# Kernel tuning notes

Hardware: AMD Instinct MI355X
Metric: run time of the kernel (lower is better)

## Reference

```python
import jax, jax.numpy as jnp
import numpy as np

N = 50000        # nodes
E = 1600000      # edges
G = 512          # graphs in batch
IN = 128         # in_dim
HID = 32         # hidden_dim
H = 4            # heads in conv1
NEG_SLOPE = 0.2  # PyG GATConv default


def setup_inputs() -> dict:
    key = jax.random.key(0)
    ks = jax.random.split(key, 20)
    s = 0.05
    return {
        "x": jax.random.normal(ks[0], (N, IN), jnp.float32),
        "edge_index": jax.random.randint(ks[1], (2, E), 0, N, dtype=jnp.int64),
        "edge_attr": jax.random.normal(ks[2], (E, 8), jnp.float32),
        "batch": jnp.sort(jax.random.randint(ks[3], (N,), 0, G, dtype=jnp.int64)),
        # conv1: in=IN, out=HID, heads=H, concat=True
        "W1": jax.random.normal(ks[4], (IN, H * HID), jnp.float32) * s,
        "a_src1": jax.random.normal(ks[5], (H, HID), jnp.float32) * s,
        "a_dst1": jax.random.normal(ks[6], (H, HID), jnp.float32) * s,
        "b1": jnp.zeros((H * HID,), jnp.float32),
        # conv2: in=H*HID, out=HID, heads=1, concat=False
        "W2": jax.random.normal(ks[7], (H * HID, HID), jnp.float32) * s,
        "a_src2": jax.random.normal(ks[8], (1, HID), jnp.float32) * s,
        "a_dst2": jax.random.normal(ks[9], (1, HID), jnp.float32) * s,
        "b2": jnp.zeros((HID,), jnp.float32),
        # classifier: HID -> HID//2 -> 1
        "Wc1": jax.random.normal(ks[10], (HID, HID // 2), jnp.float32) * s,
        "bc1": jnp.zeros((HID // 2,), jnp.float32),
        "Wc2": jax.random.normal(ks[11], (HID // 2, 1), jnp.float32) * s,
        "bc2": jnp.zeros((1,), jnp.float32),
    }


def gat_layer(x, src, dst, W, a_src, a_dst, b, heads, ch, concat, n):
    """PyG GATConv (eval mode): linear, edge-gathered additive attention,
    per-destination segment softmax, scatter-add aggregation."""
    h = (x @ W).reshape(n, heads, ch)                       # [N,H,C]
    alpha_s = jnp.sum(h * a_src, axis=-1)                   # [N,H]
    alpha_d = jnp.sum(h * a_dst, axis=-1)                   # [N,H]
    e = jax.nn.leaky_relu(alpha_s[src] + alpha_d[dst], NEG_SLOPE)  # [Etot,H]
    m = jax.lax.stop_gradient(jax.ops.segment_max(e, dst, num_segments=n))
    ex = jnp.exp(e - m[dst])
    den = jax.ops.segment_sum(ex, dst, num_segments=n)      # [N,H]
    alpha = ex / den[dst]                                   # [Etot,H]
    out = jax.ops.segment_sum(alpha[:, :, None] * h[src], dst, num_segments=n)
    out = out.reshape(n, heads * ch) if concat else out.mean(axis=1)
    return out + b


def reference(x, edge_index, edge_attr, batch,
              W1, a_src1, a_dst1, b1,
              W2, a_src2, a_dst2, b2,
              Wc1, bc1, Wc2, bc2):
    # add self-loops (PyG GATConv default)
    loop = jnp.arange(N, dtype=edge_index.dtype)
    src = jnp.concatenate([edge_index[0], loop])
    dst = jnp.concatenate([edge_index[1], loop])

    h = jax.nn.elu(gat_layer(x, src, dst, W1, a_src1, a_dst1, b1, H, HID, True, N))
    h = jax.nn.elu(gat_layer(h, src, dst, W2, a_src2, a_dst2, b2, 1, HID, False, N))

    # global mean pool over graphs
    cnt = jax.ops.segment_sum(jnp.ones((N,), h.dtype), batch, num_segments=G)
    pooled = jax.ops.segment_sum(h, batch, num_segments=G) / cnt[:, None]

    z = jax.nn.relu(pooled @ Wc1 + bc1)
    return (z @ Wc2 + bc2).squeeze(-1)   # [G]
```

## Files before the change

kernel.cpp:

```cpp
#include <hip/hip_runtime.h>
#include <math.h>

#define BUCKET_SHIFT 7
#define BUCKET_NODES (1 << BUCKET_SHIFT)
#define MAX_BUCK 512
#define PART_CHUNK 8192
#define PART_EPT 32

typedef _Float16 half4v __attribute__((ext_vector_type(4)));
typedef _Float16 half8v __attribute__((ext_vector_type(8)));

__device__ __forceinline__ float leaky02(float x){ return x > 0.f ? x : 0.2f * x; }
__device__ __forceinline__ float eluf(float x){ return x > 0.f ? x : expm1f(x); }

__global__ __launch_bounds__(256) void gemm1_hist_kernel(
    const float* __restrict__ x, const float* __restrict__ W,
    const float* __restrict__ a_src, const float* __restrict__ a_dst,
    _Float16* __restrict__ h, float* __restrict__ as_, float* __restrict__ ad_, int n,
    const int* __restrict__ dstv, int* __restrict__ bucketPartial, int pbPad,
    int E, int K, int histBlocks,
    int* __restrict__ zbase, int zwords)
{
  const int t = threadIdx.x;
  if (blockIdx.x < histBlocks) {
    __shared__ int hist[MAX_BUCK];
    for (int b = t; b < K; b += 256) hist[b] = 0;
    __syncthreads();
    const int j = blockIdx.x;
    int cbase = j * PART_CHUNK;
    for (int q = 0; q < PART_EPT; ++q) {
      int e = cbase + q * 256 + t;
      if (e < E) atomicAdd(&hist[dstv[e] >> BUCKET_SHIFT], 1);
    }
    __syncthreads();
    for (int b = t; b < K; b += 256)
      bucketPartial[(size_t)b * pbPad + j] = hist[b];
    if (j == 0) {
      for (int i = t; i < zwords; i += 256) zbase[i] = 0;
    }
    return;
  }
  const int g = blockIdx.x - histBlocks;
  const int row0 = g * 16;
  __shared__ float xs[16][128];
  __shared__ float sS[16][128];
  __shared__ float sD[16][128];
  for (int idx = t; idx < 16 * 32; idx += 256) {
    int r = idx >> 5, k4 = idx & 31;
    float4 v = (row0 + r < n) ? ((const float4*)x)[(size_t)(row0 + r) * 32 + k4]
                              : make_float4(0.f, 0.f, 0.f, 0.f);
    *(float4*)&xs[r][k4 * 4] = v;
  }
  __syncthreads();
  const int col = t & 127, hf = t >> 7;
  float acc[8] = {0,0,0,0,0,0,0,0};
  for (int k = 0; k < 128; k += 4) {
    float w0 = W[(k + 0) * 128 + col];
    float w1 = W[(k + 1) * 128 + col];
    float w2 = W[(k + 2) * 128 + col];
    float w3 = W[(k + 3) * 128 + col];
    #pragma unroll
    for (int r = 0; r < 8; ++r) {
      const float4 xv = *(const float4*)&xs[hf * 8 + r][k];
      acc[r] += xv.x * w0 + xv.y * w1 + xv.z * w2 + xv.w * w3;
    }
  }
  float asv = a_src[col], adv = a_dst[col];
  #pragma unroll
  for (int r = 0; r < 8; ++r) {
    int row = hf * 8 + r;
    float hv = acc[r];
    if (row0 + row < n) h[(size_t)(row0 + row) * 128 + col] = (_Float16)hv;
    sS[row][col] = hv * asv;
    sD[row][col] = hv * adv;
  }
  __syncthreads();
  if (t < 128) {
    int r = t >> 3, head = (t >> 1) & 3, which = t & 1;
    if (row0 + r < n) {
      const float (*buf)[128] = which ? sD : sS;
      double s2 = 0;
      for (int cc = 0; cc < 32; ++cc) s2 += (double)buf[r][head * 32 + cc];
      (which ? ad_ : as_)[(row0 + r) * 4 + head] = (float)s2;
    }
  }
}

__global__ __launch_bounds__(256) void scan_rows_kernel(
    int* __restrict__ partial, int pbPad, int* __restrict__ bucketStart, int pb)
{
  const int b = blockIdx.x;
  const int t = threadIdx.x;
  int* row = partial + (size_t)b * pbPad;
  __shared__ int s[256];
  __shared__ int carry_s;
  if (t == 0) carry_s = 0;
  __syncthreads();
  for (int base = 0; base < pb; base += 256) {
    int v = (base + t < pb) ? row[base + t] : 0;
    s[t] = v;
    __syncthreads();
    for (int off = 1; off < 256; off <<= 1) {
      int xv = (t >= off) ? s[t - off] : 0;
      __syncthreads();
      s[t] += xv;
      __syncthreads();
    }
    int incl = s[t];
    int carry = carry_s;
    if (base + t < pb) row[base + t] = carry + incl - v;
    __syncthreads();
    if (t == 255) carry_s = carry + incl;
    __syncthreads();
  }
  if (t == 0) bucketStart[b] = carry_s;
}

__global__ __launch_bounds__(256) void scan_buckets_kernel(int* __restrict__ arr, int nb) {
  __shared__ int s[256];
  __shared__ int carry_s;
  int t = threadIdx.x;
  if (t == 0) carry_s = 0;
  __syncthreads();
  for (int b = 0; b < nb; b += 256) {
    int v = (b + t < nb) ? arr[b + t] : 0;
    s[t] = v;
    __syncthreads();
    for (int off = 1; off < 256; off <<= 1) {
      int x = (t >= off) ? s[t - off] : 0;
      __syncthreads();
      s[t] += x;
      __syncthreads();
    }
    int incl = s[t];
    int carry = carry_s;
    if (b + t < nb) arr[b + t] = carry + incl - v;
    __syncthreads();
    if (t == 255) carry_s = carry + incl;
    __syncthreads();
  }
}

__global__ __launch_bounds__(256) void partition_kernel(
    const int* __restrict__ src, const int* __restrict__ dst,
    const int* __restrict__ bucketStart, const int* __restrict__ pre, int pbPad,
    unsigned int* __restrict__ bucketed, int E, int K)
{
  __shared__ int base_s[MAX_BUCK];
  __shared__ int cur[MAX_BUCK];
  const int j = blockIdx.x;
  for (int b = threadIdx.x; b < K; b += 256) {
    base_s[b] = bucketStart[b] + pre[(size_t)b * pbPad + j];
    cur[b] = 0;
  }
  __syncthreads();
  int cbase = j * PART_CHUNK;
  for (int q = 0; q < PART_EPT; ++q) {
    int e = cbase + q * 256 + threadIdx.x;
    if (e < E) {
      int d = dst[e];
      int b = d >> BUCKET_SHIFT;
      int r = atomicAdd(&cur[b], 1);
      bucketed[base_s[b] + r] =
          ((unsigned int)src[e] << BUCKET_SHIFT) | (unsigned int)(d & (BUCKET_NODES - 1));
    }
  }
}

__global__ __launch_bounds__(256) void fill_csr_kernel(
    const unsigned int* __restrict__ bucketed, const int* __restrict__ bucketStart,
    int* __restrict__ rowStart, int* __restrict__ col, int n, int E, int K)
{
  int b = blockIdx.x;
  int nodeBase = b << BUCKET_SHIFT;
  int t = threadIdx.x;
  __shared__ int hist[BUCKET_NODES];
  __shared__ int rs[BUCKET_NODES];
  __shared__ int cur[BUCKET_NODES];
  if (t < BUCKET_NODES) hist[t] = 0;
  __syncthreads();
  int bs = bucketStart[b];
  int be = (b + 1 < K) ? bucketStart[b + 1] : E;
  for (int i = bs + t; i < be; i += 256)
    atomicAdd(&hist[bucketed[i] & (BUCKET_NODES - 1)], 1);
  __syncthreads();
  if (t < BUCKET_NODES) rs[t] = hist[t];
  __syncthreads();
  for (int off = 1; off < BUCKET_NODES; off <<= 1) {
    int v = (t < BUCKET_NODES && t >= off) ? rs[t - off] : 0;
    __syncthreads();
    if (t < BUCKET_NODES) rs[t] += v;
    __syncthreads();
  }
  if (t < BUCKET_NODES) {
    int node = nodeBase + t;
    int excl = bs + rs[t] - hist[t];
    if (node < n) rowStart[node] = excl;
    rs[t] = excl;
    cur[t] = 0;
  }
  if (b == K - 1 && t == 0) rowStart[n] = E;
  __syncthreads();
  for (int i = bs + t; i < be; i += 256) {
    unsigned int rec = bucketed[i];
    int local = rec & (BUCKET_NODES - 1);
    int pos = rs[local] + atomicAdd(&cur[local], 1);
    col[pos] = (int)(rec >> BUCKET_SHIFT);
  }
}

__global__ __launch_bounds__(256) void gat_aggr1_kernel(
    const _Float16* __restrict__ feat,
    const float* __restrict__ as_,
    const float* __restrict__ ad_,
    const int* __restrict__ rowStart,
    const int* __restrict__ col,
    const float* __restrict__ bias,
    _Float16* __restrict__ out, int n)
{
  constexpr int CHUNK = 16;
  const int t    = threadIdx.x;
  const int wave = t >> 6;
  const int lane = t & 63;
  const int grp  = lane >> 4;
  const int li   = lane & 15;
  const int slot = wave * 4 + grp;
  const int node = blockIdx.x * 16 + slot;
  const int hc   = li >> 2;

  __shared__ int   s_off[16][CHUNK];
  __shared__ float s_p[16][CHUNK * 4];

  if (node >= n) return;

  const int beg = rowStart[node];
  const int deg = rowStart[node + 1] - beg;

  const float4 advv = ((const float4*)ad_)[node];
  const float4 asvv = ((const float4*)as_)[node];
  const float adv[4] = {advv.x, advv.y, advv.z, advv.w};
  float es;
  {
    float e0 = leaky02(asvv.x + adv[0]);
    float e1 = leaky02(asvv.y + adv[1]);
    float e2 = leaky02(asvv.z + adv[2]);
    float e3 = leaky02(asvv.w + adv[3]);
    es = (hc == 0) ? e0 : (hc == 1) ? e1 : (hc == 2) ? e2 : e3;
  }
  const float ps = expf(es);

  const char* featc = (const char*)feat + (li << 4);
  const half8v fself = *(const half8v*)(featc + ((size_t)node << 8));
  float accf[8];
  #pragma unroll
  for (int q = 0; q < 8; ++q) accf[q] = ps * (float)fself[q];
  float den = ps;

  int    st_s = 0;
  float4 st_q = make_float4(0.f, 0.f, 0.f, 0.f);
  if (deg > 0 && li < min(CHUNK, deg)) {
    st_s = col[beg + li];
    st_q = ((const float4*)as_)[st_s];
  }

  const int nch = (deg + CHUNK - 1) / CHUNK;
  for (int c = 0; c < nch; ++c) {
    const int base = c * CHUNK;
    const int cnt  = min(CHUNK, deg - base);
    if (li < cnt) {
      s_off[slot][li] = st_s << 8;
      float4 pp;
      pp.x = expf(leaky02(st_q.x + adv[0]));
      pp.y = expf(leaky02(st_q.y + adv[1]));
      pp.z = expf(leaky02(st_q.z + adv[2]));
      pp.w = expf(leaky02(st_q.w + adv[3]));
      *(float4*)&s_p[slot][li * 4] = pp;
    }
    __builtin_amdgcn_wave_barrier();
    const int nbase = base + CHUNK;
    if (nbase + li < deg) {
      st_s = col[beg + nbase + li];
      st_q = ((const float4*)as_)[st_s];
    }
    float a[8] = {0,0,0,0,0,0,0,0};
    float df = 0.f;
    if (cnt == CHUNK) {
      int off[16];
      #pragma unroll
      for (int j = 0; j < 16; ++j) off[j] = s_off[slot][j];
      half8v r[16];
      #pragma unroll
      for (int j = 0; j < 16; ++j) r[j] = *(const half8v*)(featc + off[j]);
      #pragma unroll
      for (int j = 0; j < 16; ++j) {
        float p = s_p[slot][j * 4 + hc];
        #pragma unroll
        for (int q = 0; q < 8; ++q) a[q] += p * (float)r[j][q];
        df += p;
      }
    } else {
      for (int j = 0; j < cnt; ++j) {
        int off = s_off[slot][j];
        float p = s_p[slot][j * 4 + hc];
        const half8v f = *(const half8v*)(featc + off);
        #pragma unroll
        for (int q = 0; q < 8; ++q) a[q] += p * (float)f[q];
        df += p;
      }
    }
    __builtin_amdgcn_wave_barrier();
    #pragma unroll
    for (int q = 0; q < 8; ++q) accf[q] += a[q];
    den += df;
  }

  const float4 bv0 = ((const float4*)bias)[2 * li];
  const float4 bv1 = ((const float4*)bias)[2 * li + 1];
  const float bb[8] = {bv0.x, bv0.y, bv0.z, bv0.w, bv1.x, bv1.y, bv1.z, bv1.w};
  const float inv = 1.0f / den;
  half8v ov;
  #pragma unroll
  for (int q = 0; q < 8; ++q)
    ov[q] = (_Float16)eluf(accf[q] * inv + bb[q]);
  *(half8v*)((char*)out + ((size_t)node << 8) + (li << 4)) = ov;
}

__global__ __launch_bounds__(128) void gemm2_kernel(
    const _Float16* __restrict__ x, const float* __restrict__ W,
    const float* __restrict__ a_src, const float* __restrict__ a_dst,
    _Float16* __restrict__ h, float* __restrict__ as_, float* __restrict__ ad_, int n)
{
  const int t = threadIdx.x;
  const int row0 = blockIdx.x * 8;
  __shared__ float xs[8][128];
  __shared__ float sH[8][32];
  for (int idx = t; idx < 8 * 16; idx += 128) {
    int r = idx >> 4, k8 = idx & 15;
    half8v v;
    #pragma unroll
    for (int q = 0; q < 8; ++q) v[q] = (_Float16)0.f;
    if (row0 + r < n) v = ((const half8v*)x)[(size_t)(row0 + r) * 16 + k8];
    #pragma unroll
    for (int q = 0; q < 8; ++q) xs[r][k8 * 8 + q] = (float)v[q];
  }
  __syncthreads();
  int col = t & 31, rp = t >> 5;
  int r0 = rp * 2, r1 = r0 + 1;
  float a0 = 0, a1 = 0;
  for (int k = 0; k < 128; k += 4) {
    float w0 = W[(k + 0) * 32 + col];
    float w1 = W[(k + 1) * 32 + col];
    float w2 = W[(k + 2) * 32 + col];
    float w3 = W[(k + 3) * 32 + col];
    float4 x0 = *(const float4*)&xs[r0][k];
    float4 x1 = *(const float4*)&xs[r1][k];
    a0 += x0.x * w0 + x0.y * w1 + x0.z * w2 + x0.w * w3;
    a1 += x1.x * w0 + x1.y * w1 + x1.z * w2 + x1.w * w3;
  }
  if (row0 + r0 < n) h[(size_t)(row0 + r0) * 32 + col] = (_Float16)a0;
  if (row0 + r1 < n) h[(size_t)(row0 + r1) * 32 + col] = (_Float16)a1;
  sH[r0][col] = a0; sH[r1][col] = a1;
  __syncthreads();
  if (t < 16) {
    int r = t >> 1, which = t & 1;
    if (row0 + r < n) {
      const float* a = which ? a_dst : a_src;
      double s = 0;
      for (int cc = 0; cc < 32; ++cc) s += (double)sH[r][cc] * (double)a[cc];
      (which ? ad_ : as_)[row0 + r] = (float)s;
    }
  }
}

__global__ __launch_bounds__(256) void gat_aggr2_kernel(
    const _Float16* __restrict__ feat,
    const float* __restrict__ as_,
    const float* __restrict__ ad_,
    const int* __restrict__ rowStart,
    const int* __restrict__ col,
    const float* __restrict__ bias,
    float* __restrict__ out, int n)
{
  constexpr int CHUNK = 16;
  const int t    = threadIdx.x;
  const int wave = t >> 6;
  const int lane = t & 63;
  const int grp  = lane >> 3;
  const int li   = lane & 7;
  const int slot = wave * 8 + grp;
  const int node = blockIdx.x * 32 + slot;

  __shared__ int   s_off[32][CHUNK];
  __shared__ float s_p[32][CHUNK];

  if (node >= n) return;

  const int beg = rowStart[node];
  const int deg = rowStart[node + 1] - beg;

  const float adv = ad_[node];
  const float ps  = expf(leaky02(as_[node] + adv));

  const char* featc = (const char*)feat + (li << 3);
  const half4v fself = *(const half4v*)(featc + ((size_t)node << 6));
  float a0s = ps * (float)fself.x;
  float a1s = ps * (float)fself.y;
  float a2s = ps * (float)fself.z;
  float a3s = ps * (float)fself.w;
  float den = ps;

  int   st_s0 = 0, st_s1 = 0;
  float st_q0 = 0.f, st_q1 = 0.f;
  if (deg > 0) {
    int c0 = min(CHUNK, deg);
    if (li < c0)     { st_s0 = col[beg + li];     st_q0 = as_[st_s0]; }
    if (li + 8 < c0) { st_s1 = col[beg + li + 8]; st_q1 = as_[st_s1]; }
  }

  const int nch = (deg + CHUNK - 1) / CHUNK;
  for (int c = 0; c < nch; ++c) {
    const int base = c * CHUNK;
    const int cnt  = min(CHUNK, deg - base);
    if (li < cnt)     { s_off[slot][li]     = st_s0 << 6; s_p[slot][li]     = expf(leaky02(st_q0 + adv)); }
    if (li + 8 < cnt) { s_off[slot][li + 8] = st_s1 << 6; s_p[slot][li + 8] = expf(leaky02(st_q1 + adv)); }
    __builtin_amdgcn_wave_barrier();
    const int nbase = base + CHUNK;
    if (nbase < deg) {
      if (nbase + li < deg)     { st_s0 = col[beg + nbase + li];     st_q0 = as_[st_s0]; }
      if (nbase + li + 8 < deg) { st_s1 = col[beg + nbase + li + 8]; st_q1 = as_[st_s1]; }
    }
    float a0 = 0.f, a1 = 0.f, a2 = 0.f, a3 = 0.f, df = 0.f;
    if (cnt == CHUNK) {
      int off[16];
      #pragma unroll
      for (int j = 0; j < 16; ++j) off[j] = s_off[slot][j];
      half4v r[16];
      #pragma unroll
      for (int j = 0; j < 16; ++j) r[j] = *(const half4v*)(featc + off[j]);
      #pragma unroll
      for (int j = 0; j < 16; ++j) {
        float p = s_p[slot][j];
        a0 += p * (float)r[j].x; a1 += p * (float)r[j].y;
        a2 += p * (float)r[j].z; a3 += p * (float)r[j].w;
        df += p;
      }
    } else {
      for (int j = 0; j < cnt; ++j) {
        int off = s_off[slot][j];
        float p = s_p[slot][j];
        const half4v f = *(const half4v*)(featc + off);
        a0 += p * (float)f.x; a1 += p * (float)f.y;
        a2 += p * (float)f.z; a3 += p * (float)f.w;
        df += p;
      }
    }
    __builtin_amdgcn_wave_barrier();
    a0s += a0; a1s += a1; a2s += a2; a3s += a3;
    den += df;
  }

  const float inv = 1.0f / den;
  const float4 bv = *(const float4*)(bias + 4 * li);
  float4 o;
  o.x = eluf(a0s * inv + bv.x);
  o.y = eluf(a1s * inv + bv.y);
  o.z = eluf(a2s * inv + bv.z);
  o.w = eluf(a3s * inv + bv.w);
  *(float4*)(out + (size_t)node * 32 + 4 * li) = o;
}

__global__ __launch_bounds__(256) void pool_kernel(const float* __restrict__ act2,
    const int* __restrict__ batch, float* __restrict__ pooled,
    float* __restrict__ cnt, int n)
{
  int t = threadIdx.x;
  int c = t & 31, r = t >> 5;
  int n0 = blockIdx.x * 64 + r * 8;
  float run = 0.f; int gcur = -1; int len = 0;
  for (int i = 0; i < 8; ++i) {
    int nd = n0 + i;
    if (nd >= n) break;
    int gb = batch[nd];
    if (gb != gcur) {
      if (gcur >= 0) {
        atomicAdd(&pooled[gcur * 32 + c], run);
        if (c == 0) atomicAdd(&cnt[gcur], (float)len);
      }
      gcur = gb; run = 0.f; len = 0;
    }
    run += act2[(size_t)nd * 32 + c];
    len++;
  }
  if (gcur >= 0) {
    atomicAdd(&pooled[gcur * 32 + c], run);
    if (c == 0) atomicAdd(&cnt[gcur], (float)len);
  }
}

__global__ void classifier_kernel(const float* __restrict__ pooled, const float* __restrict__ cnt,
    const float* __restrict__ Wc1, const float* __restrict__ bc1,
    const float* __restrict__ Wc2, const float* __restrict__ bc2,
    float* __restrict__ outp, int g_total)
{
  int g = blockIdx.x * blockDim.x + threadIdx.x;
  if (g < g_total) {
    float inv = 1.0f / cnt[g];
    float pm[32];
    for (int c = 0; c < 32; ++c) pm[c] = pooled[g * 32 + c] * inv;
    double o = (double)bc2[0];
    for (int j = 0; j < 16; ++j) {
      double z = (double)bc1[j];
      for (int c = 0; c < 32; ++c) z += (double)pm[c] * (double)Wc1[c * 16 + j];
      float zr = (float)z;
      zr = zr > 0.f ? zr : 0.f;
      o += (double)zr * (double)Wc2[j];
    }
    outp[g] = (float)o;
  }
}

extern "C" void kernel_launch(void* const* d_in, const int* in_sizes, int n_in,
                              void* d_out, int out_size, void* d_ws, size_t ws_size,
                              hipStream_t stream)
{
  const float* x      = (const float*)d_in[0];
  const int*   ei     = (const int*)d_in[1];
  const int*   batch  = (const int*)d_in[3];
  const float* W1     = (const float*)d_in[4];
  const float* a_src1 = (const float*)d_in[5];
  const float* a_dst1 = (const float*)d_in[6];
  const float* b1     = (const float*)d_in[7];
  const float* W2     = (const float*)d_in[8];
  const float* a_src2 = (const float*)d_in[9];
  const float* a_dst2 = (const float*)d_in[10];
  const float* b2     = (const float*)d_in[11];
  const float* Wc1    = (const float*)d_in[12];
  const float* bc1    = (const float*)d_in[13];
  const float* Wc2    = (const float*)d_in[14];
  const float* bc2    = (const float*)d_in[15];

  const int N = in_sizes[0] / 128;
  const int E = in_sizes[1] / 2;
  const int G = out_size;

  const int* srcv = ei;
  const int* dstv = ei + E;

  char* ws = (char*)d_ws;
  size_t off = 0;
  auto alloc = [&](size_t bytes) -> void* {
    void* p = ws + off;
    off += (bytes + 255) & ~(size_t)255;
    return p;
  };
  const int K  = (N + BUCKET_NODES - 1) >> BUCKET_SHIFT;
  const int pb = (E + PART_CHUNK - 1) / PART_CHUNK;
  const int pbPad = (pb + 63) & ~63;

  _Float16* h1   = (_Float16*)alloc((size_t)N * 128 * 2);
  _Float16* act1 = (_Float16*)alloc((size_t)N * 128 * 2);
  _Float16* h2   = (_Float16*)alloc((size_t)N * 32 * 2);
  float* act2  = (float*)alloc((size_t)N * 32 * 4);
  float* as1   = (float*)alloc((size_t)N * 4 * 4);
  float* ad1   = (float*)alloc((size_t)N * 4 * 4);
  float* as2   = (float*)alloc((size_t)N * 4);
  float* ad2   = (float*)alloc((size_t)N * 4);
  int*   rowStart = (int*)alloc((size_t)(N + 1) * 4);
  int*   colv     = (int*)alloc((size_t)E * 4);
  unsigned int* bucketed = (unsigned int*)alloc((size_t)E * 4);
  int*   bucketPartial = (int*)alloc((size_t)MAX_BUCK * pbPad * 4);
  int*   bucketStart   = (int*)alloc((size_t)MAX_BUCK * 4);
  size_t zoff0 = off;
  float* pooled = (float*)alloc((size_t)G * 32 * 4);
  float* cntG   = (float*)alloc((size_t)G * 4);
  size_t zoff1 = off;
  const int zwords = (int)((zoff1 - zoff0) / 4);
  int* zbase = (int*)pooled;

  const int gemmBlocks = (N + 15) / 16;
  gemm1_hist_kernel<<<pb + gemmBlocks, 256, 0, stream>>>(
      x, W1, a_src1, a_dst1, h1, as1, ad1, N,
      dstv, bucketPartial, pbPad, E, K, pb, zbase, zwords);
  scan_rows_kernel<<<K, 256, 0, stream>>>(bucketPartial, pbPad, bucketStart, pb);
  scan_buckets_kernel<<<1, 256, 0, stream>>>(bucketStart, K);
  partition_kernel<<<pb, 256, 0, stream>>>(srcv, dstv, bucketStart, bucketPartial, pbPad,
                                           bucketed, E, K);
  fill_csr_kernel<<<K, 256, 0, stream>>>(bucketed, bucketStart, rowStart, colv, N, E, K);
  gat_aggr1_kernel<<<(N + 15) / 16, 256, 0, stream>>>(h1, as1, ad1, rowStart, colv, b1, act1, N);
  gemm2_kernel<<<(N + 7) / 8, 128, 0, stream>>>(act1, W2, a_src2, a_dst2, h2, as2, ad2, N);
  gat_aggr2_kernel<<<(N + 31) / 32, 256, 0, stream>>>(h2, as2, ad2, rowStart, colv, b2, act2, N);
  pool_kernel<<<(N + 63) / 64, 256, 0, stream>>>(act2, batch, pooled, cntG, N);
  classifier_kernel<<<(G + 255) / 256, 256, 0, stream>>>(pooled, cntG, Wc1, bc1, Wc2, bc2,
                                                         (float*)d_out, G);
}
```

Baseline: 364.1 us.

## Fuse bucket scan into partition/fill kernels and double aggregation chunk size

Removes the single-block scan_buckets_kernel launch; each partition and fill_csr block now recomputes the exclusive scan of bucket totals in LDS. Both GAT aggregation kernels double their edge chunk from 16 to 32 and prefetch twice as many neighbor indices and attention scores per iteration. The scan change trades one serial launch for redundant per-block scan work. The larger chunk puts more gather loads in flight per step, at the cost of register and LDS pressure and more partial chunks for low-degree nodes.

```diff
diff --git a/kernel.cpp b/kernel.cpp
--- a/kernel.cpp
+++ b/kernel.cpp
@@ -12,6 +12,29 @@
 
 __device__ __forceinline__ float leaky02(float x){ return x > 0.f ? x : 0.2f * x; }
 __device__ __forceinline__ float eluf(float x){ return x > 0.f ? x : expm1f(x); }
+
+__device__ __forceinline__ void lds_exclusive_scan(int* sc, int K, int* s, int* carry_s) {
+  const int t = threadIdx.x;
+  if (t == 0) *carry_s = 0;
+  __syncthreads();
+  for (int base = 0; base < K; base += 256) {
+    int v = (base + t < K) ? sc[base + t] : 0;
+    s[t] = v;
+    __syncthreads();
+    for (int off = 1; off < 256; off <<= 1) {
+      int xv = (t >= off) ? s[t - off] : 0;
+      __syncthreads();
+      s[t] += xv;
+      __syncthreads();
+    }
+    int incl = s[t];
+    int carry = *carry_s;
+    if (base + t < K) sc[base + t] = carry + incl - v;
+    __syncthreads();
+    if (t == 255) *carry_s = carry + incl;
+    __syncthreads();
+  }
+}
 
 __global__ __launch_bounds__(256) void gemm1_hist_kernel(
     const float* __restrict__ x, const float* __restrict__ W,
@@ -87,7 +110,7 @@
 }
 
 __global__ __launch_bounds__(256) void scan_rows_kernel(
-    int* __restrict__ partial, int pbPad, int* __restrict__ bucketStart, int pb)
+    int* __restrict__ partial, int pbPad, int* __restrict__ bucketTotal, int pb)
 {
   const int b = blockIdx.x;
   const int t = threadIdx.x;
@@ -113,50 +136,32 @@
     if (t == 255) carry_s = carry + incl;
     __syncthreads();
   }
-  if (t == 0) bucketStart[b] = carry_s;
-}
-
-__global__ __launch_bounds__(256) void scan_buckets_kernel(int* __restrict__ arr, int nb) {
+  if (t == 0) bucketTotal[b] = carry_s;
+}
+
+__global__ __launch_bounds__(256) void partition_kernel(
+    const int* __restrict__ src, const int* __restrict__ dst,
+    const int* __restrict__ bucketTotal, const int* __restrict__ pre, int pbPad,
+    unsigned int* __restrict__ bucketed, int E, int K)
+{
+  __shared__ int sc[MAX_BUCK];
   __shared__ int s[256];
   __shared__ int carry_s;
-  int t = threadIdx.x;
-  if (t == 0) carry_s = 0;
-  __syncthreads();
-  for (int b = 0; b < nb; b += 256) {
-    int v = (b + t < nb) ? arr[b + t] : 0;
-    s[t] = v;
-    __syncthreads();
-    for (int off = 1; off < 256; off <<= 1) {
-      int x = (t >= off) ? s[t - off] : 0;
-      __syncthreads();
-      s[t] += x;
-      __syncthreads();
-    }
-    int incl = s[t];
-    int carry = carry_s;
-    if (b + t < nb) arr[b + t] = carry + incl - v;
-    __syncthreads();
-    if (t == 255) carry_s = carry + incl;
-    __syncthreads();
-  }
-}
-
-__global__ __launch_bounds__(256) void partition_kernel(
-    const int* __restrict__ src, const int* __restrict__ dst,
-    const int* __restrict__ bucketStart, const int* __restrict__ pre, int pbPad,
-    unsigned int* __restrict__ bucketed, int E, int K)
-{
   __shared__ int base_s[MAX_BUCK];
   __shared__ int cur[MAX_BUCK];
+  const int t = threadIdx.x;
   const int j = blockIdx.x;
-  for (int b = threadIdx.x; b < K; b += 256) {
-    base_s[b] = bucketStart[b] + pre[(size_t)b * pbPad + j];
+  for (int b = t; b < K; b += 256) sc[b] = bucketTotal[b];
+  __syncthreads();
+  lds_exclusive_scan(sc, K, s, &carry_s);
+  for (int b = t; b < K; b += 256) {
+    base_s[b] = sc[b] + pre[(size_t)b * pbPad + j];
     cur[b] = 0;
   }
   __syncthreads();
   int cbase = j * PART_CHUNK;
   for (int q = 0; q < PART_EPT; ++q) {
-    int e = cbase + q * 256 + threadIdx.x;
+    int e = cbase + q * 256 + t;
     if (e < E) {
       int d = dst[e];
       int b = d >> BUCKET_SHIFT;
@@ -168,19 +173,24 @@
 }
 
 __global__ __launch_bounds__(256) void fill_csr_kernel(
-    const unsigned int* __restrict__ bucketed, const int* __restrict__ bucketStart,
+    const unsigned int* __restrict__ bucketed, const int* __restrict__ bucketTotal,
     int* __restrict__ rowStart, int* __restrict__ col, int n, int E, int K)
 {
   int b = blockIdx.x;
   int nodeBase = b << BUCKET_SHIFT;
   int t = threadIdx.x;
+  __shared__ int sc[MAX_BUCK];
+  __shared__ int s[256];
+  __shared__ int carry_s;
   __shared__ int hist[BUCKET_NODES];
   __shared__ int rs[BUCKET_NODES];
   __shared__ int cur[BUCKET_NODES];
+  for (int bb = t; bb < K; bb += 256) sc[bb] = bucketTotal[bb];
   if (t < BUCKET_NODES) hist[t] = 0;
   __syncthreads();
-  int bs = bucketStart[b];
-  int be = (b + 1 < K) ? bucketStart[b + 1] : E;
+  lds_exclusive_scan(sc, K, s, &carry_s);
+  int bs = sc[b];
+  int be = (b + 1 < K) ? sc[b + 1] : E;
   for (int i = bs + t; i < be; i += 256)
     atomicAdd(&hist[bucketed[i] & (BUCKET_NODES - 1)], 1);
   __syncthreads();
@@ -218,7 +228,7 @@
     const float* __restrict__ bias,
     _Float16* __restrict__ out, int n)
 {
-  constexpr int CHUNK = 16;
+  constexpr int CHUNK = 32;
   const int t    = threadIdx.x;
   const int wave = t >> 6;
   const int lane = t & 63;
@@ -256,11 +266,13 @@
   for (int q = 0; q < 8; ++q) accf[q] = ps * (float)fself[q];
   float den = ps;
 
-  int    st_s = 0;
-  float4 st_q = make_float4(0.f, 0.f, 0.f, 0.f);
-  if (deg > 0 && li < min(CHUNK, deg)) {
-    st_s = col[beg + li];
-    st_q = ((const float4*)as_)[st_s];
+  int    st_s0 = 0, st_s1 = 0;
+  float4 st_q0 = make_float4(0.f, 0.f, 0.f, 0.f);
+  float4 st_q1 = make_float4(0.f, 0.f, 0.f, 0.f);
+  if (deg > 0) {
+    int c0 = min(CHUNK, deg);
+    if (li < c0)      { st_s0 = col[beg + li];      st_q0 = ((const float4*)as_)[st_s0]; }
+    if (li + 16 < c0) { st_s1 = col[beg + li + 16]; st_q1 = ((const float4*)as_)[st_s1]; }
   }
 
   const int nch = (deg + CHUNK - 1) / CHUNK;
@@ -268,35 +280,51 @@
     const int base = c * CHUNK;
     const int cnt  = min(CHUNK, deg - base);
     if (li < cnt) {
-      s_off[slot][li] = st_s << 8;
+      s_off[slot][li] = st_s0 << 8;
       float4 pp;
-      pp.x = expf(leaky02(st_q.x + adv[0]));
-      pp.y = expf(leaky02(st_q.y + adv[1]));
-      pp.z = expf(leaky02(st_q.z + adv[2]));
-      pp.w = expf(leaky02(st_q.w + adv[3]));
+      pp.x = expf(leaky02(st_q0.x + adv[0]));
+      pp.y = expf(leaky02(st_q0.y + adv[1]));
+      pp.z = expf(leaky02(st_q0.z + adv[2]));
+      pp.w = expf(leaky02(st_q0.w + adv[3]));
       *(float4*)&s_p[slot][li * 4] = pp;
+    }
+    if (li + 16 < cnt) {
+      s_off[slot][li + 16] = st_s1 << 8;
+      float4 pp;
+      pp.x = expf(leaky02(st_q1.x + adv[0]));
+      pp.y = expf(leaky02(st_q1.y + adv[1]));
+      pp.z = expf(leaky02(st_q1.z + adv[2]));
+      pp.w = expf(leaky02(st_q1.w + adv[3]));
+      *(float4*)&s_p[slot][(li + 16) * 4] = pp;
     }
     __builtin_amdgcn_wave_barrier();
     const int nbase = base + CHUNK;
     if (nbase + li < deg) {
-      st_s = col[beg + nbase + li];
-      st_q = ((const float4*)as_)[st_s];
+      st_s0 = col[beg + nbase + li];
+      st_q0 = ((const float4*)as_)[st_s0];
+    }
+    if (nbase + li + 16 < deg) {
+      st_s1 = col[beg + nbase + li + 16];
+      st_q1 = ((const float4*)as_)[st_s1];
     }
     float a[8] = {0,0,0,0,0,0,0,0};
     float df = 0.f;
     if (cnt == CHUNK) {
-      int off[16];
       #pragma unroll
-      for (int j = 0; j < 16; ++j) off[j] = s_off[slot][j];
-      half8v r[16];
-      #pragma unroll
-      for (int j = 0; j < 16; ++j) r[j] = *(const half8v*)(featc + off[j]);
-      #pragma unroll
-      for (int j = 0; j < 16; ++j) {
-        float p = s_p[slot][j * 4 + hc];
+      for (int half = 0; half < 2; ++half) {
+        int off[16];
         #pragma unroll
-        for (int q = 0; q < 8; ++q) a[q] += p * (float)r[j][q];
-        df += p;
+        for (int j = 0; j < 16; ++j) off[j] = s_off[slot][half * 16 + j];
+        half8v r[16];
+        #pragma unroll
+        for (int j = 0; j < 16; ++j) r[j] = *(const half8v*)(featc + off[j]);
+        #pragma unroll
+        for (int j = 0; j < 16; ++j) {
+          float p = s_p[slot][(half * 16 + j) * 4 + hc];
+          #pragma unroll
+          for (int q = 0; q < 8; ++q) a[q] += p * (float)r[j][q];
+          df += p;
+        }
       }
     } else {
       for (int j = 0; j < cnt; ++j) {
@@ -381,7 +409,7 @@
     const float* __restrict__ bias,
     float* __restrict__ out, int n)
 {
-  constexpr int CHUNK = 16;
+  constexpr int CHUNK = 32;
   const int t    = threadIdx.x;
   const int wave = t >> 6;
   const int lane = t & 63;
@@ -409,40 +437,49 @@
   float a3s = ps * (float)fself.w;
   float den = ps;
 
-  int   st_s0 = 0, st_s1 = 0;
-  float st_q0 = 0.f, st_q1 = 0.f;
+  int   st_s0 = 0, st_s1 = 0, st_s2 = 0, st_s3 = 0;
+  float st_q0 = 0.f, st_q1 = 0.f, st_q2 = 0.f, st_q3 = 0.f;
   if (deg > 0) {
     int c0 = min(CHUNK, deg);
-    if (li < c0)     { st_s0 = col[beg + li];     st_q0 = as_[st_s0]; }
-    if (li + 8 < c0) { st_s1 = col[beg + li + 8]; st_q1 = as_[st_s1]; }
+    if (li < c0)      { st_s0 = col[beg + li];      st_q0 = as_[st_s0]; }
+    if (li + 8 < c0)  { st_s1 = col[beg + li + 8];  st_q1 = as_[st_s1]; }
+    if (li + 16 < c0) { st_s2 = col[beg + li + 16]; st_q2 = as_[st_s2]; }
+    if (li + 24 < c0) { st_s3 = col[beg + li + 24]; st_q3 = as_[st_s3]; }
   }
 
   const int nch = (deg + CHUNK - 1) / CHUNK;
   for (int c = 0; c < nch; ++c) {
     const int base = c * CHUNK;
     const int cnt  = min(CHUNK, deg - base);
-    if (li < cnt)     { s_off[slot][li]     = st_s0 << 6; s_p[slot][li]     = expf(leaky02(st_q0 + adv)); }
-    if (li + 8 < cnt) { s_off[slot][li + 8] = st_s1 << 6; s_p[slot][li + 8] = expf(leaky02(st_q1 + adv)); }
+    if (li < cnt)      { s_off[slot][li]      = st_s0 << 6; s_p[slot][li]      = expf(leaky02(st_q0 + adv)); }
+    if (li + 8 < cnt)  { s_off[slot][li + 8]  = st_s1 << 6; s_p[slot][li + 8]  = expf(leaky02(st_q1 + adv)); }
+    if (li + 16 < cnt) { s_off[slot][li + 16] = st_s2 << 6; s_p[slot][li + 16] = expf(leaky02(st_q2 + adv)); }
+    if (li + 24 < cnt) { s_off[slot][li + 24] = st_s3 << 6; s_p[slot][li + 24] = expf(leaky02(st_q3 + adv)); }
     __builtin_amdgcn_wave_barrier();
     const int nbase = base + CHUNK;
     if (nbase < deg) {
-      if (nbase + li < deg)     { st_s0 = col[beg + nbase + li];     st_q0 = as_[st_s0]; }
-      if (nbase + li + 8 < deg) { st_s1 = col[beg + nbase + li + 8]; st_q1 = as_[st_s1]; }
+      if (nbase + li < deg)      { st_s0 = col[beg + nbase + li];      st_q0 = as_[st_s0]; }
+      if (nbase + li + 8 < deg)  { st_s1 = col[beg + nbase + li + 8];  st_q1 = as_[st_s1]; }
+      if (nbase + li + 16 < deg) { st_s2 = col[beg + nbase + li + 16]; st_q2 = as_[st_s2]; }
+      if (nbase + li + 24 < deg) { st_s3 = col[beg + nbase + li + 24]; st_q3 = as_[st_s3]; }
     }
     float a0 = 0.f, a1 = 0.f, a2 = 0.f, a3 = 0.f, df = 0.f;
     if (cnt == CHUNK) {
-      int off[16];
       #pragma unroll
-      for (int j = 0; j < 16; ++j) off[j] = s_off[slot][j];
-      half4v r[16];
-      #pragma unroll
-      for (int j = 0; j < 16; ++j) r[j] = *(const half4v*)(featc + off[j]);
-      #pragma unroll
-      for (int j = 0; j < 16; ++j) {
-        float p = s_p[slot][j];
-        a0 += p * (float)r[j].x; a1 += p * (float)r[j].y;
-        a2 += p * (float)r[j].z; a3 += p * (float)r[j].w;
-        df += p;
+      for (int half = 0; half < 2; ++half) {
+        int off[16];
+        #pragma unroll
+        for (int j = 0; j < 16; ++j) off[j] = s_off[slot][half * 16 + j];
+        half4v r[16];
+        #pragma unroll
+        for (int j = 0; j < 16; ++j) r[j] = *(const half4v*)(featc + off[j]);
+        #pragma unroll
+        for (int j = 0; j < 16; ++j) {
+          float p = s_p[slot][half * 16 + j];
+          a0 += p * (float)r[j].x; a1 += p * (float)r[j].y;
+          a2 += p * (float)r[j].z; a3 += p * (float)r[j].w;
+          df += p;
+        }
       }
     } else {
       for (int j = 0; j < cnt; ++j) {
@@ -569,7 +606,7 @@
   int*   colv     = (int*)alloc((size_t)E * 4);
   unsigned int* bucketed = (unsigned int*)alloc((size_t)E * 4);
   int*   bucketPartial = (int*)alloc((size_t)MAX_BUCK * pbPad * 4);
-  int*   bucketStart   = (int*)alloc((size_t)MAX_BUCK * 4);
+  int*   bucketTotal   = (int*)alloc((size_t)MAX_BUCK * 4);
   size_t zoff0 = off;
   float* pooled = (float*)alloc((size_t)G * 32 * 4);
   float* cntG   = (float*)alloc((size_t)G * 4);
@@ -581,11 +618,10 @@
   gemm1_hist_kernel<<<pb + gemmBlocks, 256, 0, stream>>>(
       x, W1, a_src1, a_dst1, h1, as1, ad1, N,
       dstv, bucketPartial, pbPad, E, K, pb, zbase, zwords);
-  scan_rows_kernel<<<K, 256, 0, stream>>>(bucketPartial, pbPad, bucketStart, pb);
-  scan_buckets_kernel<<<1, 256, 0, stream>>>(bucketStart, K);
-  partition_kernel<<<pb, 256, 0, stream>>>(srcv, dstv, bucketStart, bucketPartial, pbPad,
+  scan_rows_kernel<<<K, 256, 0, stream>>>(bucketPartial, pbPad, bucketTotal, pb);
+  partition_kernel<<<pb, 256, 0, stream>>>(srcv, dstv, bucketTotal, bucketPartial, pbPad,
                                            bucketed, E, K);
-  fill_csr_kernel<<<K, 256, 0, stream>>>(bucketed, bucketStart, rowStart, colv, N, E, K);
+  fill_csr_kernel<<<K, 256, 0, stream>>>(bucketed, bucketTotal, rowStart, colv, N, E, K);
   gat_aggr1_kernel<<<(N + 15) / 16, 256, 0, stream>>>(h1, as1, ad1, rowStart, colv, b1, act1, N);
   gemm2_kernel<<<(N + 7) / 8, 128, 0, stream>>>(act1, W2, a_src2, a_dst2, h2, as2, ad2, N);
   gat_aggr2_kernel<<<(N + 31) / 32, 256, 0, stream>>>(h2, as2, ad2, rowStart, colv, b2, act2, N);
```

Result: slower. 382.7 us (+5.1%).
